# Performance work log

Measured on AMD Instinct MI355X. Metric: run time of the kernel, lower is better.

## Reference

```python
import jax, jax.numpy as jnp
import numpy as np

N = [100000, 25000, 6250]        # nodes per scale (coarsening pyramid)
F = 128                          # features_per_scale (all equal)
H = 4                            # num_heads (only enters via the score scale)
SCALE = float((F // H) ** 0.5)
OUT = 5                          # out_channels
E_SAME = [1000000, 400000, 100000]
E_INC = [400000, 100000]


def _cross_attn(src, dst, src_feat, n_dst, qW, qb, kW, kb, vW, vb):
    # GAT-style gather -> per-edge score -> segment softmax over dst -> scatter.
    # In the original model dst_feat is zeros, so Q = 0 @ qW + qb; we keep the
    # matmul so qW appears in the autodiff graph (its grad is zero, faithfully).
    K = src_feat @ kW + kb
    V = src_feat @ vW + vb
    Q = jnp.zeros((n_dst, qW.shape[1]), src_feat.dtype) @ qW + qb
    score = (Q[dst] * K[src]).sum(-1) / SCALE            # [E]
    m = jax.ops.segment_max(score, dst, num_segments=n_dst)
    e = jnp.exp(score - m[dst])
    denom = jax.ops.segment_sum(e, dst, num_segments=n_dst)
    attn = e / denom[dst]                                # segment softmax
    return jax.ops.segment_sum(attn[:, None] * V[src], dst, num_segments=n_dst)


def _gcn(src, dst, x, n, W, b):
    # DGL GraphConv, norm='both': D_out^-1/2 -> scatter-sum -> D_in^-1/2 -> linear.
    ones = jnp.ones(src.shape[0], x.dtype)
    deg_out = jnp.clip(jax.ops.segment_sum(ones, src, num_segments=n), 1.0)
    deg_in = jnp.clip(jax.ops.segment_sum(ones, dst, num_segments=n), 1.0)
    h = x * jax.lax.rsqrt(deg_out)[:, None]
    agg = jax.ops.segment_sum(h[src], dst, num_segments=n)
    return (agg * jax.lax.rsqrt(deg_in)[:, None]) @ W + b


def setup_inputs() -> dict:
    key = jax.random.key(0)
    cnt = [0]
    def rkey():
        cnt[0] += 1
        return jax.random.fold_in(key, cnt[0])
    def rn(shape, s=0.05):
        return jax.random.normal(rkey(), shape, jnp.float32) * s
    def ri(n, hi):
        return jax.random.randint(rkey(), (n,), 0, hi, jnp.int32)
    return {
        "X": rn((N[0], F), 1.0),
        "emb_W": rn((F, F)), "emb_b": rn((F,)),
        "gcn_W": rn((3, F, F)), "gcn_b": rn((3, F)),
        "enc_qW": rn((2, F, F)), "enc_qb": rn((2, F)),
        "enc_kW": rn((2, F, F)), "enc_kb": rn((2, F)),
        "enc_vW": rn((2, F, F)), "enc_vb": rn((2, F)),
        "dec_qW": rn((2, F, F)), "dec_qb": rn((2, F)),
        "dec_kW": rn((2, F, F)), "dec_kb": rn((2, F)),
        "dec_vW": rn((2, F, F)), "dec_vb": rn((2, F)),
        "head_W": rn((3, 2 * F, OUT)), "head_b": rn((3, OUT)),
        "g0_src": ri(E_SAME[0], N[0]), "g0_dst": ri(E_SAME[0], N[0]),
        "g1_src": ri(E_SAME[1], N[1]), "g1_dst": ri(E_SAME[1], N[1]),
        "g2_src": ri(E_SAME[2], N[2]), "g2_dst": ri(E_SAME[2], N[2]),
        "inc0_src": ri(E_INC[0], N[0]), "inc0_dst": ri(E_INC[0], N[1]),
        "inc1_src": ri(E_INC[1], N[1]), "inc1_dst": ri(E_INC[1], N[2]),
        "dec0_src": ri(E_INC[1], N[2]), "dec0_dst": ri(E_INC[1], N[1]),
        "dec1_src": ri(E_INC[0], N[1]), "dec1_dst": ri(E_INC[0], N[0]),
    }


def reference(X, emb_W, emb_b, gcn_W, gcn_b,
              enc_qW, enc_qb, enc_kW, enc_kb, enc_vW, enc_vb,
              dec_qW, dec_qb, dec_kW, dec_kb, dec_vW, dec_vb,
              head_W, head_b,
              g0_src, g0_dst, g1_src, g1_dst, g2_src, g2_dst,
              inc0_src, inc0_dst, inc1_src, inc1_dst,
              dec0_src, dec0_dst, dec1_src, dec1_dst):
    h0 = X @ emb_W + emb_b                               # embedding, scale 0
    # encoder: scale 0 -> 1 -> 2
    e1 = _cross_attn(inc0_src, inc0_dst, h0, N[1],
                     enc_qW[0], enc_qb[0], enc_kW[0], enc_kb[0], enc_vW[0], enc_vb[0])
    e2 = _cross_attn(inc1_src, inc1_dst, e1, N[2],
                     enc_qW[1], enc_qb[1], enc_kW[1], enc_kb[1], enc_vW[1], enc_vb[1])
    feats = [h0, e1, e2]
    edges = [(g0_src, g0_dst), (g1_src, g1_dst), (g2_src, g2_dst)]
    gcn_out = [_gcn(s, d, feats[i], N[i], gcn_W[i], gcn_b[i])
               for i, (s, d) in enumerate(edges)]
    # decoder: scale 2 -> 1 -> 0
    d1 = _cross_attn(dec0_src, dec0_dst, gcn_out[2], N[1],
                     dec_qW[0], dec_qb[0], dec_kW[0], dec_kb[0], dec_vW[0], dec_vb[0])
    d0 = _cross_attn(dec1_src, dec1_dst, d1, N[0],
                     dec_qW[1], dec_qb[1], dec_kW[1], dec_kb[1], dec_vW[1], dec_vb[1])
    decoded = [d0, d1, gcn_out[2]]
    outs = [jax.nn.softmax(jnp.concatenate([gcn_out[i], decoded[i]], -1) @ head_W[i] + head_b[i], -1)
            for i in range(3)]
    return jnp.concatenate(outs, 0)                      # [N0+N1+N2, OUT]
```

## Files before the change

### kernel.cpp

```cpp
#include <hip/hip_runtime.h>
#include <math.h>

#define N0 100000
#define N1 25000
#define N2 6250
#define FD 128

typedef unsigned short u16;
typedef unsigned int u32;

static inline int ceildiv(int a, int b){ return (a + b - 1)/b; }

__device__ __forceinline__ u16 f2bf(float f){
  u32 u = __float_as_uint(f);
  u += 0x7fffu + ((u >> 16) & 1u);
  return (u16)(u >> 16);
}
__device__ __forceinline__ float bf2f(u16 h){
  return __uint_as_float(((u32)h) << 16);
}
__device__ __forceinline__ float blo(u32 u){ return __uint_as_float(u << 16); }
__device__ __forceinline__ float bhi(u32 u){ return __uint_as_float(u & 0xffff0000u); }
__device__ __forceinline__ u32 pk2(float a, float b){ return (u32)f2bf(a) | ((u32)f2bf(b) << 16); }

struct BMeta {
  const int* src[7]; const int* dst[7];
  int* rowp[7]; int* csr[7];
  int* degp[7];
  int n[7], E[7], B[7], r[7];
  int eoff[8];
  int boff[8];
  int pblk[8];
};

__device__ __forceinline__ void mm_inner(const float* Al, const float* Wl, int r0, int c0, float acc[4][4]){
  #pragma unroll
  for (int kq = 0; kq < 8; ++kq) {
    int k0 = kq*4;
    float4 a[4], w[4];
    #pragma unroll
    for (int i=0;i<4;++i) a[i] = *(const float4*)&Al[(r0+i)*32 + k0];
    #pragma unroll
    for (int kk=0;kk<4;++kk) w[kk] = *(const float4*)&Wl[(k0+kk)*128 + c0];
    #pragma unroll
    for (int i=0;i<4;++i){
      acc[i][0] = fmaf(a[i].x,w[0].x, fmaf(a[i].y,w[1].x, fmaf(a[i].z,w[2].x, fmaf(a[i].w,w[3].x, acc[i][0]))));
      acc[i][1] = fmaf(a[i].x,w[0].y, fmaf(a[i].y,w[1].y, fmaf(a[i].z,w[2].y, fmaf(a[i].w,w[3].y, acc[i][1]))));
      acc[i][2] = fmaf(a[i].x,w[0].z, fmaf(a[i].y,w[1].z, fmaf(a[i].z,w[2].z, fmaf(a[i].w,w[3].z, acc[i][2]))));
      acc[i][3] = fmaf(a[i].x,w[0].w, fmaf(a[i].y,w[1].w, fmaf(a[i].z,w[2].w, fmaf(a[i].w,w[3].w, acc[i][3]))));
    }
  }
}

template<int SCORE, int SCALEDEG, int AB16>
__device__ __forceinline__ void dev_gemm(float* Wl, float* Al, int bid,
    const void* __restrict__ Ap, const int* __restrict__ deg,
    const float* __restrict__ W, const float* __restrict__ bias,
    const float* __restrict__ kvec, float* __restrict__ sOut,
    u16* __restrict__ out, int n)
{
  const int tid = threadIdx.x;
  const int row0 = bid * 32;
  const int c0 = (tid & 31) * 4, r0 = (tid >> 5) * 4;
  const int r = tid >> 3, fc = tid & 7;
  const int gr_s = row0 + r;
  float acc[4][4] = {};
  float sacc = 0.f;
  const float4* W4 = (const float4*)W;
  for (int kp = 0; kp < 4; ++kp) {
    float4* Wl4 = (float4*)Wl;
    #pragma unroll
// ... 18 lines not shown
    mm_inner(Al, Wl, r0, c0, acc);
    __syncthreads();
  }
  if (SCORE){
    sacc += __shfl_xor(sacc, 1);
    sacc += __shfl_xor(sacc, 2);
    sacc += __shfl_xor(sacc, 4);
    if (fc == 0 && gr_s < n) sOut[gr_s] = expf(sacc + kvec[128]);
  }
  float4 bv = make_float4(0.f,0.f,0.f,0.f);
  if (bias) bv = *(const float4*)&bias[c0];
  #pragma unroll
  for (int i=0;i<4;++i){
    int gr = row0 + r0 + i;
    if (gr < n){
      float rs = 1.f;
      if (SCALEDEG) rs = rsqrtf(fmaxf((float)deg[gr], 1.f));
      ushort4 o;
      o.x = f2bf(acc[i][0]*rs+bv.x); o.y = f2bf(acc[i][1]*rs+bv.y);
      o.z = f2bf(acc[i][2]*rs+bv.z); o.w = f2bf(acc[i][3]*rs+bv.w);
      *(ushort4*)&out[(size_t)gr*FD + c0] = o;
    }
  }
}

template<int AB16>
__device__ __forceinline__ void dev_dualgemm(float* sm, int bid,
    const void* __restrict__ Ap, const int* __restrict__ deg,
    const float* __restrict__ Wv, const float* __restrict__ vb,
    const float* __restrict__ Wg,
    const float* __restrict__ kvec, float* __restrict__ sOut,
    u16* __restrict__ Vout, u16* __restrict__ Yout, int n)
{
  float* WvL = sm; float* WgL = sm + 4096; float* Al = sm + 8192;
  const int tid = threadIdx.x;
  const int row0 = bid * 32;
  const int c0 = (tid & 31) * 4, r0 = (tid >> 5) * 4;
  const int r = tid >> 3, fc = tid & 7;
  const int gr_s = row0 + r;
  float accV[4][4] = {};
  float accY[4][4] = {};
  float sacc = 0.f;
  const float4* Wv4 = (const float4*)Wv;
// ... 23 lines not shown
    __syncthreads();
  }
  sacc += __shfl_xor(sacc, 1);
  sacc += __shfl_xor(sacc, 2);
  sacc += __shfl_xor(sacc, 4);
  if (fc == 0 && gr_s < n) sOut[gr_s] = expf(sacc + kvec[128]);
  float4 bv = *(const float4*)&vb[c0];
  #pragma unroll
  for (int i=0;i<4;++i){
    int gr = row0 + r0 + i;
    if (gr < n){
      ushort4 o;
      o.x = f2bf(accV[i][0]+bv.x); o.y = f2bf(accV[i][1]+bv.y);
      o.z = f2bf(accV[i][2]+bv.z); o.w = f2bf(accV[i][3]+bv.w);
      *(ushort4*)&Vout[(size_t)gr*FD + c0] = o;
      float rs = rsqrtf(fmaxf((float)deg[gr], 1.f));
      ushort4 y;
      y.x = f2bf(accY[i][0]*rs); y.y = f2bf(accY[i][1]*rs);
      y.z = f2bf(accY[i][2]*rs); y.w = f2bf(accY[i][3]*rs);
      *(ushort4*)&Yout[(size_t)gr*FD + c0] = y;
    }
  }
}

__device__ __forceinline__ void dev_p0(const BMeta& m, int bid, int* __restrict__ bktCnt, int* sh){
  int j = 0;
  #pragma unroll
  for (int t = 1; t < 7; ++t) if (bid >= m.pblk[t]) j = t;
  int lb = bid - m.pblk[j];
  const int* dst = m.dst[j]; const int* src = m.src[j];
  int* dp = m.degp[j];
  int E = m.E[j], r = m.r[j], B = m.B[j];
  if (threadIdx.x < 64) sh[threadIdx.x] = 0;
  __syncthreads();
  int base = lb*4096 + threadIdx.x;
  #pragma unroll
  for (int i = 0; i < 16; ++i){
    int e = base + i*256;
    if (e < E){
      atomicAdd(&sh[dst[e]/r], 1);
      if (dp) atomicAdd(&dp[src[e]], 1);
    }
  }
  __syncthreads();
  if ((int)threadIdx.x < B) atomicAdd(&bktCnt[m.boff[j] + threadIdx.x], sh[threadIdx.x]);
}

__device__ __forceinline__ void dev_p1(const BMeta& m, const int* __restrict__ bktCnt,
    int* __restrict__ bktBase, int* __restrict__ bktCur, int* sh){
  int tid = threadIdx.x;
  if (tid < 224) sh[tid] = bktCnt[tid];
  __syncthreads();
  if (tid < 7){
    int acc = m.eoff[tid];
    for (int b = m.boff[tid]; b < m.boff[tid+1]; ++b){ int v = sh[b]; sh[b] = acc; acc += v; }
  }
  __syncthreads();
  if (tid < 224){ bktBase[tid] = sh[tid]; bktCur[tid] = sh[tid]; }
}

__device__ __forceinline__ void dev_p2(const BMeta& m, int bid, int* __restrict__ bktCur,
    u32* __restrict__ ebuf, int* sh){
  int j = 0;
  #pragma unroll
  for (int t = 1; t < 7; ++t) if (bid >= m.pblk[t]) j = t;
  int lb = bid - m.pblk[j];
  const int* src = m.src[j]; const int* dst = m.dst[j];
  int E = m.E[j], r = m.r[j], B = m.B[j];
  int* h = sh; int* start = sh + 64;
  if (threadIdx.x < 64) h[threadIdx.x] = 0;
  __syncthreads();
  int base = lb*4096 + threadIdx.x;
  #pragma unroll
  for (int i = 0; i < 16; ++i){ int e = base + i*256; if (e < E) atomicAdd(&h[dst[e]/r], 1); }
  __syncthreads();
  if ((int)threadIdx.x < B) start[threadIdx.x] = atomicAdd(&bktCur[m.boff[j] + threadIdx.x], h[threadIdx.x]);
  __syncthreads();
  #pragma unroll
  for (int i = 0; i < 16; ++i){
    int e = base + i*256;
    if (e < E){
      int s = src[e], d = dst[e];
      int b = d / r;
      int pos = atomicAdd(&start[b], 1);
      ebuf[pos] = ((u32)(d - b*r) << 17) | (u32)s;
    }
  }
}

__device__ __forceinline__ void dev_p3(const BMeta& m, int bb,
    const int* __restrict__ bktCnt, const int* __restrict__ bktBase,
    const u32* __restrict__ ebuf, int* sh){
  int j = 0;
  #pragma unroll
  for (int t = 1; t < 7; ++t) if (bb >= m.boff[t]) j = t;
  int b = bb - m.boff[j];
  int n = m.n[j], r = m.r[j], B = m.B[j];
  int* rowp = m.rowp[j]; int* csr = m.csr[j];
  int node0 = b*r;
  int rr = min(r, n - node0);
  int gbase = bktBase[bb];
  int cnt = bktCnt[bb];
  int lbase = gbase - m.eoff[j];
  int* hist = sh; int* aux = sh + 1568;
  int tid = threadIdx.x;
  for (int i = tid; i < rr; i += 256) hist[i] = 0;
  __syncthreads();
  for (int e = tid; e < cnt; e += 256){ u32 pk = ebuf[gbase + e]; atomicAdd(&hist[pk >> 17], 1); }
  __syncthreads();
  int ch = (rr + 255) >> 8;
  int i0 = tid*ch;
  int s = 0;
  for (int k = 0; k < ch; ++k){ int idx = i0 + k; if (idx < rr){ int t = hist[idx]; hist[idx] = s; s += t; } }
  aux[tid] = s; __syncthreads();
  for (int off = 1; off < 256; off <<= 1){
    int v = aux[tid]; int a = (tid >= off) ? aux[tid - off] : 0;
    __syncthreads();
    aux[tid] = v + a;
    __syncthreads();
  }
// ... 38 lines not shown
    a0*=inv; a1*=inv; a2*=inv; a3*=inv; a4*=inv; a5*=inv; a6*=inv; a7*=inv;
  }
  if (OB16){
    uint4 o; o.x = pk2(a0,a1); o.y = pk2(a2,a3); o.z = pk2(a4,a5); o.w = pk2(a6,a7);
    ((uint4*)out)[(size_t)row*16 + lane] = o;
  } else {
    float4* o4 = (float4*)out;
    o4[(size_t)row*32 + lane*2]     = make_float4(a0,a1,a2,a3);
    o4[(size_t)row*32 + lane*2 + 1] = make_float4(a4,a5,a6,a7);
  }
}

template<int OB16>
__device__ __forceinline__ void dev_gcn_gather16(int bid,
    const int* __restrict__ csr, const int* __restrict__ rowp,
    const u16* __restrict__ Y, const float* __restrict__ bias,
    void* __restrict__ out, int n)
{
  int g = threadIdx.x >> 4, lane = threadIdx.x & 15;
  int row = bid*16 + g;
  if (row >= n) return;
  int st = rowp[row], en = rowp[row+1];
  float a0=0,a1=0,a2=0,a3=0,a4=0,a5=0,a6=0,a7=0;
  const uint4* Y8 = (const uint4*)Y;
  for (int e = st; e < en; ++e){
    int sn = csr[e];
    uint4 v = Y8[(size_t)sn*16 + lane];
    a0 += blo(v.x); a1 += bhi(v.x);
    a2 += blo(v.y); a3 += bhi(v.y);
    a4 += blo(v.z); a5 += bhi(v.z);
    a6 += blo(v.w); a7 += bhi(v.w);
  }
  float sc = rsqrtf(fmaxf((float)(en - st), 1.f));
  const float4* b4 = (const float4*)bias;
  float4 ba = b4[lane*2], bb = b4[lane*2+1];
  float o0=fmaf(a0,sc,ba.x), o1=fmaf(a1,sc,ba.y), o2=fmaf(a2,sc,ba.z), o3=fmaf(a3,sc,ba.w);
  float o4v=fmaf(a4,sc,bb.x), o5=fmaf(a5,sc,bb.y), o6=fmaf(a6,sc,bb.z), o7=fmaf(a7,sc,bb.w);
  if (OB16){
    uint4 o; o.x = pk2(o0,o1); o.y = pk2(o2,o3); o.z = pk2(o4v,o5); o.w = pk2(o6,o7);
    ((uint4*)out)[(size_t)row*16 + lane] = o;
  } else {
    float4* o4 = (float4*)out;
    o4[(size_t)row*32 + lane*2]     = make_float4(o0,o1,o2,o3);
    o4[(size_t)row*32 + lane*2 + 1] = make_float4(o4v,o5,o6,o7);
  }
}
// ... 58 lines not shown
      }
    }
  } else {
    int i = (bid-4)*256 + threadIdx.x;
    if (i < ntot) zeroBlk[i] = 0;
  }
}

__global__ __launch_bounds__(256) void k2_p0_gemm(BMeta m, int* __restrict__ bktCnt,
    const float* __restrict__ X, const float* __restrict__ W, const float* __restrict__ b,
    u16* __restrict__ bh0, int np0)
{
  __shared__ float sm[5120];
  int bid = blockIdx.x;
  if (bid < np0) dev_p0(m, bid, bktCnt, (int*)sm);
  else dev_gemm<0,0,0>(sm, sm+4096, bid - np0, X, nullptr, W, b, nullptr, nullptr, bh0, N0);
}

__global__ __launch_bounds__(256) void k3_p1(BMeta m,
    const int* __restrict__ bktCnt, int* __restrict__ bktBase, int* __restrict__ bktCur)
{
  __shared__ int sh[256];
  dev_p1(m, bktCnt, bktBase, bktCur, sh);
}

__global__ __launch_bounds__(256) void k4_p2_dual(BMeta m, int* __restrict__ bktCur, u32* __restrict__ ebuf,
    const u16* __restrict__ bh0, const int* __restrict__ deg0,
    const float* __restrict__ evW, const float* __restrict__ evb, const float* __restrict__ gW,
    const float* __restrict__ kvec, float* __restrict__ sS, u16* __restrict__ bV, u16* __restrict__ bY0,
    int np2, int gOff)
{
  __shared__ float sm[9216];
  int bid = blockIdx.x;
  if (bid < np2) dev_p2(m, bid, bktCur, ebuf, (int*)sm);
  else dev_dualgemm<1>(sm, gOff + bid - np2, bh0, deg0, evW, evb, gW, kvec, sS, bV, bY0, N0);
}

__global__ __launch_bounds__(256) void k5_p3_dual(BMeta m,
    const int* __restrict__ bktCnt, const int* __restrict__ bktBase, const u32* __restrict__ ebuf,
    const u16* __restrict__ bh0, const int* __restrict__ deg0,
    const float* __restrict__ evW, const float* __restrict__ evb, const float* __restrict__ gW,
    const float* __restrict__ kvec, float* __restrict__ sS, u16* __restrict__ bV, u16* __restrict__ bY0,
    int np3, int gOff)
{
  __shared__ float sm[9216];
  int bid = blockIdx.x;
  if (bid < np3) dev_p3(m, bid, bktCnt, bktBase, ebuf, (int*)sm);
  else dev_dualgemm<1>(sm, gOff + bid - np3, bh0, deg0, evW, evb, gW, kvec, sS, bV, bY0, N0);
}

__global__ __launch_bounds__(256) void k6_ag_i0(
    const int* __restrict__ csrA, const int* __restrict__ rowpA,
    const float* __restrict__ sS, const u16* __restrict__ bV, u16* __restrict__ be1,
    const int* __restrict__ csr0, const int* __restrict__ rowp0, const u16* __restrict__ bY0,
    const float* __restrict__ gb, u16* __restrict__ bg0, int nMain, int sBase)
{
  int bid = blockIdx.x;
  if (bid < nMain) dev_attn_gather16<1>(bid, csrA, rowpA, sS, bV, be1, N1);
  else dev_gcn_gather16<1>(sBase + bid - nMain, csr0, rowp0, bY0, gb, bg0, N0);
}

__global__ __launch_bounds__(256) void k7_dual_enc1(
    const u16* __restrict__ be1, const int* __restrict__ deg1,
    const float* __restrict__ vW, const float* __restrict__ vb, const float* __restrict__ gW,
    const float* __restrict__ kvec, float* __restrict__ sS, u16* __restrict__ bV, u16* __restrict__ bY1,
    const int* __restrict__ csr0, const int* __restrict__ rowp0, const u16* __restrict__ bY0,
    const float* __restrict__ gb, u16* __restrict__ bg0, int nMain, int sBase)
{
  __shared__ float sm[9216];
  int bid = blockIdx.x;
  if (bid < nMain) dev_dualgemm<1>(sm, bid, be1, deg1, vW, vb, gW, kvec, sS, bV, bY1, N1);
  else dev_gcn_gather16<1>(sBase + bid - nMain, csr0, rowp0, bY0, gb, bg0, N0);
}

__global__ __launch_bounds__(256) void k8_ag_i1(
    const int* __restrict__ csrA, const int* __restrict__ rowpA,
    const float* __restrict__ sS, const u16* __restrict__ bV, float* __restrict__ be2,
    const int* __restrict__ csr0, const int* __restrict__ rowp0, const u16* __restrict__ bY0,
    const float* __restrict__ gb, u16* __restrict__ bg0, int nMain, int sBase)
{
  int bid = blockIdx.x;
  if (bid < nMain) dev_attn_gather16<0>(bid, csrA, rowpA, sS, bV, be2, N2);
  else dev_gcn_gather16<1>(sBase + bid - nMain, csr0, rowp0, bY0, gb, bg0, N0);
}

__global__ __launch_bounds__(256) void k9_y2_g1(
    const float* __restrict__ be2, const int* __restrict__ deg2, const float* __restrict__ W2, u16* __restrict__ bY2,
    const int* __restrict__ csr1, const int* __restrict__ rowp1, const u16* __restrict__ bY1,
    const float* __restrict__ b1, u16* __restrict__ bg1,
    const int* __restrict__ csr0, const int* __restrict__ rowp0, const u16* __restrict__ bY0,
    const float* __restrict__ gb, u16* __restrict__ bg0, int ngemm, int nMain, int sBase)
{
  __shared__ float sm[5120];
  int bid = blockIdx.x;
  if (bid < ngemm) dev_gemm<0,1,0>(sm, sm+4096, bid, be2, deg2, W2, nullptr, nullptr, nullptr, bY2, N2);
  else if (bid < nMain) dev_gcn_gather16<1>(bid - ngemm, csr1, rowp1, bY1, b1, bg1, N1);
  else dev_gcn_gather16<1>(sBase + bid - nMain, csr0, rowp0, bY0, gb, bg0, N0);
}

__global__ __launch_bounds__(256) void k10_g2(
    const int* __restrict__ csr2, const int* __restrict__ rowp2, const u16* __restrict__ bY2,
    const float* __restrict__ b2, float* __restrict__ bg2,
    const int* __restrict__ csr0, const int* __restrict__ rowp0, const u16* __restrict__ bY0,
    const float* __restrict__ gb, u16* __restrict__ bg0, int nMain, int sBase)
{
  int bid = blockIdx.x;
  if (bid < nMain) dev_gcn_gather16<0>(bid, csr2, rowp2, bY2, b2, bg2, N2);
  else dev_gcn_gather16<1>(sBase + bid - nMain, csr0, rowp0, bY0, gb, bg0, N0);
}

__global__ __launch_bounds__(256) void k11_dec0_head2(
    const float* __restrict__ bg2, const float* __restrict__ vW, const float* __restrict__ vb,
    const float* __restrict__ kvec, float* __restrict__ sS, u16* __restrict__ bV,
    const float* __restrict__ hW, const float* __restrict__ hb, float* __restrict__ out,
    const int* __restrict__ csr0, const int* __restrict__ rowp0, const u16* __restrict__ bY0,
    const float* __restrict__ gb, u16* __restrict__ bg0, int ngemm, int nMain, int sBase)
{
  __shared__ float sm[5120];
  int bid = blockIdx.x;
  if (bid < ngemm) dev_gemm<1,0,0>(sm, sm+4096, bid, bg2, nullptr, vW, vb, kvec, sS, bV, N2);
  else if (bid < nMain) dev_head<0,0>(bid - ngemm, bg2, bg2, hW, hb, out, N2, N0+N1);
  else dev_gcn_gather16<1>(sBase + bid - nMain, csr0, rowp0, bY0, gb, bg0, N0);
}

__global__ __launch_bounds__(256) void k12_ag_d1(
    const int* __restrict__ csrA, const int* __restrict__ rowpA,
    const float* __restrict__ sS, const u16* __restrict__ bV, u16* __restrict__ be1,
    const int* __restrict__ csr0, const int* __restrict__ rowp0, const u16* __restrict__ bY0,
    const float* __restrict__ gb, u16* __restrict__ bg0, int nMain, int sBase)
{
  int bid = blockIdx.x;
  if (bid < nMain) dev_attn_gather16<1>(bid, csrA, rowpA, sS, bV, be1, N1);
  else dev_gcn_gather16<1>(sBase + bid - nMain, csr0, rowp0, bY0, gb, bg0, N0);
}

__global__ __launch_bounds__(256) void k13_dec1_head1(
    const u16* __restrict__ be1, const float* __restrict__ vW, const float* __restrict__ vb,
    const float* __restrict__ kvec, float* __restrict__ sS, u16* __restrict__ bV,
    const u16* __restrict__ bg1, const float* __restrict__ hW, const float* __restrict__ hb,
    float* __restrict__ out,
    const int* __restrict__ csr0, const int* __restrict__ rowp0, const u16* __restrict__ bY0,
    const float* __restrict__ gb, u16* __restrict__ bg0, int ngemm, int nMain, int sBase)
{
  __shared__ float sm[5120];
  int bid = blockIdx.x;
  if (bid < ngemm) dev_gemm<1,0,1>(sm, sm+4096, bid, be1, nullptr, vW, vb, kvec, sS, bV, N1);
  else if (bid < nMain) dev_head<1,1>(bid - ngemm, bg1, be1, hW, hb, out, N1, N0);
  else dev_gcn_gather16<1>(sBase + bid - nMain, csr0, rowp0, bY0, gb, bg0, N0);
}

__global__ __launch_bounds__(256) void k14_gather_head0(
    const int* __restrict__ csr, const int* __restrict__ rowp,
    const float* __restrict__ w, const u16* __restrict__ V,
    const u16* __restrict__ bg0,
    const float* __restrict__ hW, const float* __restrict__ hb,
    float* __restrict__ out)
{
  int g = threadIdx.x >> 4, lane = threadIdx.x & 15;
  int row = blockIdx.x*16 + g;
  if (row >= N0) return;
  int st = rowp[row], en = rowp[row+1];
  float a0=0,a1=0,a2=0,a3=0,a4=0,a5=0,a6=0,a7=0;
  if (en > st){
// ... 71 lines not shown
  const int* g2d  = (const int*)d_in[24];
  const int* i0s  = (const int*)d_in[25];
  const int* i0d  = (const int*)d_in[26];
  const int* i1s  = (const int*)d_in[27];
  const int* i1d  = (const int*)d_in[28];
  const int* dc0s = (const int*)d_in[29];
  const int* dc0d = (const int*)d_in[30];
  const int* dc1s = (const int*)d_in[31];
  const int* dc1d = (const int*)d_in[32];

  float* ws = (float*)d_ws;
  float* sS  = ws;
  float* kvec = sS + N0;
  float* be2 = kvec + 4*132;
  float* bg2 = be2 + (size_t)N2*FD;
  u16*  bh0 = (u16*)(bg2 + (size_t)N2*FD);
  u16*  be1 = bh0 + (size_t)N0*FD;
  u16*  bg0 = be1 + (size_t)N1*FD;
  u16*  bg1 = bg0 + (size_t)N0*FD;
  u16*  bV  = bg1 + (size_t)N1*FD;
  u16*  bY0 = bV  + (size_t)N0*FD;
  u16*  bY1 = bV + 4000000;
  u16*  bY2 = bV + 8000000;
  int*  degBlk  = (int*)(bY0 + (size_t)N0*FD);
  int*  bktCnt  = degBlk + (N0+N1+N2);
  int*  bktBase = bktCnt + 224;
  int*  bktCur  = bktBase + 224;
  int*  rowpBlk = bktCur + 224;
  int*  csrBlk  = rowpBlk + 287507;
  u32*  ebuf    = (u32*)(csrBlk + 2500000);

  const int* srcP[7] = {g0s,g1s,g2s,i0s,i1s,dc0s,dc1s};
  const int* dstP[7] = {g0d,g1d,g2d,i0d,i1d,dc0d,dc1d};
  const int nArr[7] = {N0,N1,N2,N1,N2,N1,N0};
  const int EArr[7] = {1000000,400000,100000,400000,100000,100000,400000};
  const int BArr[7] = {64,32,8,32,8,16,64};
  const int rArr[7] = {1563,782,782,782,782,1563,1563};
  int* deg0 = degBlk; int* deg1 = degBlk + N0; int* deg2 = degBlk + N0 + N1;
  int* degP[7] = {deg0, deg1, deg2, nullptr, nullptr, nullptr, nullptr};

  BMeta m;
  {
    int eo=0, bo=0, po=0, ro=0, co=0;
    for (int j=0;j<7;++j){
      m.src[j]=srcP[j]; m.dst[j]=dstP[j]; m.degp[j]=degP[j];
      m.rowp[j]=rowpBlk+ro; m.csr[j]=csrBlk+co;
      m.n[j]=nArr[j]; m.E[j]=EArr[j]; m.B[j]=BArr[j]; m.r[j]=rArr[j];
      m.eoff[j]=eo; m.boff[j]=bo; m.pblk[j]=po;
      eo+=EArr[j]; bo+=BArr[j]; po+=ceildiv(EArr[j],4096); ro+=nArr[j]+1; co+=EArr[j];
    }
    m.eoff[7]=eo; m.boff[7]=bo; m.pblk[7]=po;
  }

  const float invScale = 0.17677669529663687f;
  float* out = (float*)d_out;

  const int NP0 = m.pblk[7];
  const int NP3 = m.boff[7];
  const int ZTOT = (N0+N1+N2) + 224;
  const int GH0 = ceildiv(N0,32);
  const int GH1 = ceildiv(N1,32);
  const int GH2 = ceildiv(N2,32);
  const int GS1 = 1250;
  const int GA1_16 = ceildiv(N1,16);
  const int GA2_16 = ceildiv(N2,16);
  const int G0B16  = ceildiv(N0,16);
  const int GH2H = ceildiv(N2,4);
  const int GH1H = ceildiv(N1,4);

  int ss[9];
  for (int i = 0; i <= 8; ++i) ss[i] = (int)(((long long)G0B16 * i) / 8);

  k1_zero_kqv<<<4 + ceildiv(ZTOT,256), 256, 0, stream>>>(degBlk, ZTOT,
      enc_kW, enc_kb, enc_qb, dec_kW, dec_kb, dec_qb, kvec, invScale);
  k2_p0_gemm<<<NP0 + GH0, 256, 0, stream>>>(m, bktCnt, X, emb_W, emb_b, bh0, NP0);
  k3_p1<<<1, 256, 0, stream>>>(m, bktCnt, bktBase, bktCur);
  k4_p2_dual<<<NP0 + GS1, 256, 0, stream>>>(m, bktCur, ebuf,
      bh0, deg0, enc_vW, enc_vb, gcn_W, kvec, sS, bV, bY0, NP0, 0);
  k5_p3_dual<<<NP3 + (GH0 - GS1), 256, 0, stream>>>(m, bktCnt, bktBase, ebuf,
      bh0, deg0, enc_vW, enc_vb, gcn_W, kvec, sS, bV, bY0, NP3, GS1);
  k6_ag_i0<<<GA1_16 + (ss[1]-ss[0]), 256, 0, stream>>>(m.csr[3], m.rowp[3], sS, bV, be1,
      m.csr[0], m.rowp[0], bY0, gcn_b, bg0, GA1_16, ss[0]);
  k7_dual_enc1<<<GH1 + (ss[2]-ss[1]), 256, 0, stream>>>(be1, deg1,
      enc_vW+16384, enc_vb+128, gcn_W+16384, kvec+132, sS, bV, bY1,
      m.csr[0], m.rowp[0], bY0, gcn_b, bg0, GH1, ss[1]);
  k8_ag_i1<<<GA2_16 + (ss[3]-ss[2]), 256, 0, stream>>>(m.csr[4], m.rowp[4], sS, bV, be2,
      m.csr[0], m.rowp[0], bY0, gcn_b, bg0, GA2_16, ss[2]);
  k9_y2_g1<<<GH2 + GA1_16 + (ss[4]-ss[3]), 256, 0, stream>>>(be2, deg2, gcn_W+32768, bY2,
      m.csr[1], m.rowp[1], bY1, gcn_b+128, bg1,
      m.csr[0], m.rowp[0], bY0, gcn_b, bg0, GH2, GH2+GA1_16, ss[3]);
  k10_g2<<<GA2_16 + (ss[5]-ss[4]), 256, 0, stream>>>(m.csr[2], m.rowp[2], bY2, gcn_b+256, bg2,
      m.csr[0], m.rowp[0], bY0, gcn_b, bg0, GA2_16, ss[4]);
  k11_dec0_head2<<<GH2 + GH2H + (ss[6]-ss[5]), 256, 0, stream>>>(bg2, dec_vW, dec_vb, kvec+264, sS, bV,
      head_W+2560, head_b+10, out,
      m.csr[0], m.rowp[0], bY0, gcn_b, bg0, GH2, GH2+GH2H, ss[5]);
  k12_ag_d1<<<GA1_16 + (ss[7]-ss[6]), 256, 0, stream>>>(m.csr[5], m.rowp[5], sS, bV, be1,
      m.csr[0], m.rowp[0], bY0, gcn_b, bg0, GA1_16, ss[6]);
  k13_dec1_head1<<<GH1 + GH1H + (ss[8]-ss[7]), 256, 0, stream>>>(be1, dec_vW+16384, dec_vb+128, kvec+396, sS, bV,
      bg1, head_W+1280, head_b+5, out,
      m.csr[0], m.rowp[0], bY0, gcn_b, bg0, GH1, GH1+GH1H, ss[7]);
  k14_gather_head0<<<G0B16, 256, 0, stream>>>(m.csr[6], m.rowp[6], sS, bV, bg0,
      head_W, head_b, out);
}
```

Measured before the change: 471.6 us.

## Compute out-degree via bucketed shared histograms and apply D_out scaling during GCN gather

Out-degree counting used to rely on global atomicAdd per edge into a degree array. It now reuses the bucket-sort machinery: source keys are binned into 16-bit local indices, and per-bucket shared-memory histograms write rsqrt(out-degree) directly. The GEMM epilogues no longer scale Y by out-degree. Instead the GCN gather multiplies each neighbour row by rs[src] with an FMA, which adds one scalar load per edge. This adds extra binning passes over three edge lists and more scratch buffers, in exchange for removing contended global atomics.

Measured after the change: 457.1 us. -3.1%, faster.

```diff
diff --git a/kernel.cpp b/kernel.cpp
--- a/kernel.cpp
+++ b/kernel.cpp
@@ -24,13 +24,15 @@
 __device__ __forceinline__ u32 pk2(float a, float b){ return (u32)f2bf(a) | ((u32)f2bf(b) << 16); }
 
 struct BMeta {
-  const int* src[7]; const int* dst[7];
+  const int* key[10];
+  const int* src[7];
   int* rowp[7]; int* csr[7];
-  int* degp[7];
-  int n[7], E[7], B[7], r[7];
+  float* rsout[3];
+  int n[10], E[10], B[10], r[10];
   int eoff[8];
-  int boff[8];
-  int pblk[8];
+  int soff[4];
+  int boff[11];
+  int pblk[11];
 };
 
 __device__ __forceinline__ void mm_inner(const float* Al, const float* Wl, int r0, int c0, float acc[4][4]){
@@ -52,9 +54,9 @@
   }
 }
 
-template<int SCORE, int SCALEDEG, int AB16>
+template<int SCORE, int AB16>
 __device__ __forceinline__ void dev_gemm(float* Wl, float* Al, int bid,
-    const void* __restrict__ Ap, const int* __restrict__ deg,
+    const void* __restrict__ Ap,
     const float* __restrict__ W, const float* __restrict__ bias,
     const float* __restrict__ kvec, float* __restrict__ sOut,
     u16* __restrict__ out, int n)
@@ -103,11 +105,9 @@
   for (int i=0;i<4;++i){
     int gr = row0 + r0 + i;
     if (gr < n){
-      float rs = 1.f;
-      if (SCALEDEG) rs = rsqrtf(fmaxf((float)deg[gr], 1.f));
       ushort4 o;
-      o.x = f2bf(acc[i][0]*rs+bv.x); o.y = f2bf(acc[i][1]*rs+bv.y);
-      o.z = f2bf(acc[i][2]*rs+bv.z); o.w = f2bf(acc[i][3]*rs+bv.w);
+      o.x = f2bf(acc[i][0]+bv.x); o.y = f2bf(acc[i][1]+bv.y);
+      o.z = f2bf(acc[i][2]+bv.z); o.w = f2bf(acc[i][3]+bv.w);
       *(ushort4*)&out[(size_t)gr*FD + c0] = o;
     }
   }
@@ -115,7 +115,7 @@
 
 template<int AB16>
 __device__ __forceinline__ void dev_dualgemm(float* sm, int bid,
-    const void* __restrict__ Ap, const int* __restrict__ deg,
+    const void* __restrict__ Ap,
     const float* __restrict__ Wv, const float* __restrict__ vb,
     const float* __restrict__ Wg,
     const float* __restrict__ kvec, float* __restrict__ sOut,
@@ -169,34 +169,30 @@
       o.x = f2bf(accV[i][0]+bv.x); o.y = f2bf(accV[i][1]+bv.y);
       o.z = f2bf(accV[i][2]+bv.z); o.w = f2bf(accV[i][3]+bv.w);
       *(ushort4*)&Vout[(size_t)gr*FD + c0] = o;
-      float rs = rsqrtf(fmaxf((float)deg[gr], 1.f));
       ushort4 y;
-      y.x = f2bf(accY[i][0]*rs); y.y = f2bf(accY[i][1]*rs);
-      y.z = f2bf(accY[i][2]*rs); y.w = f2bf(accY[i][3]*rs);
+      y.x = f2bf(accY[i][0]); y.y = f2bf(accY[i][1]);
+      y.z = f2bf(accY[i][2]); y.w = f2bf(accY[i][3]);
       *(ushort4*)&Yout[(size_t)gr*FD + c0] = y;
     }
   }
 }
 
+__device__ __forceinline__ int job_of_blk(const BMeta& m, int bid){
+  int j = 0;
+  #pragma unroll
+  for (int t = 1; t < 10; ++t) if (bid >= m.pblk[t]) j = t;
+  return j;
+}
+
 __device__ __forceinline__ void dev_p0(const BMeta& m, int bid, int* __restrict__ bktCnt, int* sh){
-  int j = 0;
-  #pragma unroll
-  for (int t = 1; t < 7; ++t) if (bid >= m.pblk[t]) j = t;
+  int j = job_of_blk(m, bid);
   int lb = bid - m.pblk[j];
-  const int* dst = m.dst[j]; const int* src = m.src[j];
-  int* dp = m.degp[j];
-  int E = m.E[j], r = m.r[j], B = m.B[j];
+  const int* key = m.key[j]; int E = m.E[j], r = m.r[j], B = m.B[j];
   if (threadIdx.x < 64) sh[threadIdx.x] = 0;
   __syncthreads();
   int base = lb*4096 + threadIdx.x;
   #pragma unroll
-  for (int i = 0; i < 16; ++i){
-    int e = base + i*256;
-    if (e < E){
-      atomicAdd(&sh[dst[e]/r], 1);
-      if (dp) atomicAdd(&dp[src[e]], 1);
-    }
-  }
+  for (int i = 0; i < 16; ++i){ int e = base + i*256; if (e < E) atomicAdd(&sh[key[e]/r], 1); }
   __syncthreads();
   if ((int)threadIdx.x < B) atomicAdd(&bktCnt[m.boff[j] + threadIdx.x], sh[threadIdx.x]);
 }
@@ -204,61 +200,84 @@
 __device__ __forceinline__ void dev_p1(const BMeta& m, const int* __restrict__ bktCnt,
     int* __restrict__ bktBase, int* __restrict__ bktCur, int* sh){
   int tid = threadIdx.x;
-  if (tid < 224) sh[tid] = bktCnt[tid];
-  __syncthreads();
-  if (tid < 7){
-    int acc = m.eoff[tid];
+  for (int i = tid; i < 328; i += 256) sh[i] = bktCnt[i];
+  __syncthreads();
+  if (tid < 10){
+    int acc = (tid < 7) ? m.eoff[tid] : m.soff[tid-7];
     for (int b = m.boff[tid]; b < m.boff[tid+1]; ++b){ int v = sh[b]; sh[b] = acc; acc += v; }
   }
   __syncthreads();
-  if (tid < 224){ bktBase[tid] = sh[tid]; bktCur[tid] = sh[tid]; }
+  for (int i = tid; i < 328; i += 256){ bktBase[i] = sh[i]; bktCur[i] = sh[i]; }
 }
 
 __device__ __forceinline__ void dev_p2(const BMeta& m, int bid, int* __restrict__ bktCur,
-    u32* __restrict__ ebuf, int* sh){
-  int j = 0;
-  #pragma unroll
-  for (int t = 1; t < 7; ++t) if (bid >= m.pblk[t]) j = t;
+    u32* __restrict__ ebuf, u16* __restrict__ ebuf16, int* sh){
+  int j = job_of_blk(m, bid);
   int lb = bid - m.pblk[j];
-  const int* src = m.src[j]; const int* dst = m.dst[j];
+  const int* key = m.key[j];
   int E = m.E[j], r = m.r[j], B = m.B[j];
   int* h = sh; int* start = sh + 64;
   if (threadIdx.x < 64) h[threadIdx.x] = 0;
   __syncthreads();
   int base = lb*4096 + threadIdx.x;
   #pragma unroll
-  for (int i = 0; i < 16; ++i){ int e = base + i*256; if (e < E) atomicAdd(&h[dst[e]/r], 1); }
+  for (int i = 0; i < 16; ++i){ int e = base + i*256; if (e < E) atomicAdd(&h[key[e]/r], 1); }
   __syncthreads();
   if ((int)threadIdx.x < B) start[threadIdx.x] = atomicAdd(&bktCur[m.boff[j] + threadIdx.x], h[threadIdx.x]);
   __syncthreads();
-  #pragma unroll
-  for (int i = 0; i < 16; ++i){
-    int e = base + i*256;
-    if (e < E){
-      int s = src[e], d = dst[e];
-      int b = d / r;
-      int pos = atomicAdd(&start[b], 1);
-      ebuf[pos] = ((u32)(d - b*r) << 17) | (u32)s;
+  if (j < 7){
+    const int* src = m.src[j];
+    #pragma unroll
+    for (int i = 0; i < 16; ++i){
+      int e = base + i*256;
+      if (e < E){
+        int s = src[e], d = key[e];
+        int b = d / r;
+        int pos = atomicAdd(&start[b], 1);
+        ebuf[pos] = ((u32)(d - b*r) << 17) | (u32)s;
+      }
+    }
+  } else {
+    #pragma unroll
+    for (int i = 0; i < 16; ++i){
+      int e = base + i*256;
+      if (e < E){
+        int k = key[e];
+        int b = k / r;
+        int pos = atomicAdd(&start[b], 1);
+        ebuf16[pos] = (u16)(k - b*r);
+      }
     }
   }
 }
 
 __device__ __forceinline__ void dev_p3(const BMeta& m, int bb,
     const int* __restrict__ bktCnt, const int* __restrict__ bktBase,
-    const u32* __restrict__ ebuf, int* sh){
+    const u32* __restrict__ ebuf, const u16* __restrict__ ebuf16, int* sh){
   int j = 0;
   #pragma unroll
-  for (int t = 1; t < 7; ++t) if (bb >= m.boff[t]) j = t;
+  for (int t = 1; t < 10; ++t) if (bb >= m.boff[t]) j = t;
   int b = bb - m.boff[j];
-  int n = m.n[j], r = m.r[j], B = m.B[j];
-  int* rowp = m.rowp[j]; int* csr = m.csr[j];
+  int n = m.n[j], r = m.r[j];
   int node0 = b*r;
   int rr = min(r, n - node0);
   int gbase = bktBase[bb];
   int cnt = bktCnt[bb];
+  int tid = threadIdx.x;
+  if (j >= 7){
+    int* hist = sh;
+    for (int i = tid; i < rr; i += 256) hist[i] = 0;
+    __syncthreads();
+    for (int e = tid; e < cnt; e += 256) atomicAdd(&hist[ebuf16[gbase + e]], 1);
+    __syncthreads();
+    float* rs = m.rsout[j-7];
+    for (int i = tid; i < rr; i += 256) rs[node0 + i] = rsqrtf(fmaxf((float)hist[i], 1.f));
+    return;
+  }
+  int B = m.B[j];
+  int* rowp = m.rowp[j]; int* csr = m.csr[j];
   int lbase = gbase - m.eoff[j];
   int* hist = sh; int* aux = sh + 1568;
-  int tid = threadIdx.x;
   for (int i = tid; i < rr; i += 256) hist[i] = 0;
   __syncthreads();
   for (int e = tid; e < cnt; e += 256){ u32 pk = ebuf[gbase + e]; atomicAdd(&hist[pk >> 17], 1); }
@@ -327,8 +346,8 @@
 template<int OB16>
 __device__ __forceinline__ void dev_gcn_gather16(int bid,
     const int* __restrict__ csr, const int* __restrict__ rowp,
-    const u16* __restrict__ Y, const float* __restrict__ bias,
-    void* __restrict__ out, int n)
+    const float* __restrict__ rs, const u16* __restrict__ Y,
+    const float* __restrict__ bias, void* __restrict__ out, int n)
 {
   int g = threadIdx.x >> 4, lane = threadIdx.x & 15;
   int row = bid*16 + g;
@@ -338,11 +357,12 @@
   const uint4* Y8 = (const uint4*)Y;
   for (int e = st; e < en; ++e){
     int sn = csr[e];
+    float x = rs[sn];
     uint4 v = Y8[(size_t)sn*16 + lane];
-    a0 += blo(v.x); a1 += bhi(v.x);
-    a2 += blo(v.y); a3 += bhi(v.y);
-    a4 += blo(v.z); a5 += bhi(v.z);
-    a6 += blo(v.w); a7 += bhi(v.w);
+    a0 = fmaf(x, blo(v.x), a0); a1 = fmaf(x, bhi(v.x), a1);
+    a2 = fmaf(x, blo(v.y), a2); a3 = fmaf(x, bhi(v.y), a3);
+    a4 = fmaf(x, blo(v.z), a4); a5 = fmaf(x, bhi(v.z), a5);
+    a6 = fmaf(x, blo(v.w), a6); a7 = fmaf(x, bhi(v.w), a7);
   }
   float sc = rsqrtf(fmaxf((float)(en - st), 1.f));
   const float4* b4 = (const float4*)bias;
@@ -431,124 +451,128 @@
   __shared__ float sm[5120];
   int bid = blockIdx.x;
   if (bid < np0) dev_p0(m, bid, bktCnt, (int*)sm);
-  else dev_gemm<0,0,0>(sm, sm+4096, bid - np0, X, nullptr, W, b, nullptr, nullptr, bh0, N0);
+  else dev_gemm<0,0>(sm, sm+4096, bid - np0, X, W, b, nullptr, nullptr, bh0, N0);
 }
 
 __global__ __launch_bounds__(256) void k3_p1(BMeta m,
     const int* __restrict__ bktCnt, int* __restrict__ bktBase, int* __restrict__ bktCur)
 {
-  __shared__ int sh[256];
+  __shared__ int sh[384];
   dev_p1(m, bktCnt, bktBase, bktCur, sh);
 }
 
-__global__ __launch_bounds__(256) void k4_p2_dual(BMeta m, int* __restrict__ bktCur, u32* __restrict__ ebuf,
-    const u16* __restrict__ bh0, const int* __restrict__ deg0,
+__global__ __launch_bounds__(256) void k4_p2_dual(BMeta m, int* __restrict__ bktCur,
+    u32* __restrict__ ebuf, u16* __restrict__ ebuf16,
+    const u16* __restrict__ bh0,
     const float* __restrict__ evW, const float* __restrict__ evb, const float* __restrict__ gW,
     const float* __restrict__ kvec, float* __restrict__ sS, u16* __restrict__ bV, u16* __restrict__ bY0,
     int np2, int gOff)
 {
   __shared__ float sm[9216];
   int bid = blockIdx.x;
-  if (bid < np2) dev_p2(m, bid, bktCur, ebuf, (int*)sm);
-  else dev_dualgemm<1>(sm, gOff + bid - np2, bh0, deg0, evW, evb, gW, kvec, sS, bV, bY0, N0);
+  if (bid < np2) dev_p2(m, bid, bktCur, ebuf, ebuf16, (int*)sm);
+  else dev_dualgemm<1>(sm, gOff + bid - np2, bh0, evW, evb, gW, kvec, sS, bV, bY0, N0);
 }
 
 __global__ __launch_bounds__(256) void k5_p3_dual(BMeta m,
-    const int* __restrict__ bktCnt, const int* __restrict__ bktBase, const u32* __restrict__ ebuf,
-    const u16* __restrict__ bh0, const int* __restrict__ deg0,
+    const int* __restrict__ bktCnt, const int* __restrict__ bktBase,
+    const u32* __restrict__ ebuf, const u16* __restrict__ ebuf16,
+    const u16* __restrict__ bh0,
     const float* __restrict__ evW, const float* __restrict__ evb, const float* __restrict__ gW,
     const float* __restrict__ kvec, float* __restrict__ sS, u16* __restrict__ bV, u16* __restrict__ bY0,
     int np3, int gOff)
 {
   __shared__ float sm[9216];
   int bid = blockIdx.x;
-  if (bid < np3) dev_p3(m, bid, bktCnt, bktBase, ebuf, (int*)sm);
-  else dev_dualgemm<1>(sm, gOff + bid - np3, bh0, deg0, evW, evb, gW, kvec, sS, bV, bY0, N0);
+  if (bid < np3) dev_p3(m, bid, bktCnt, bktBase, ebuf, ebuf16, (int*)sm);
+  else dev_dualgemm<1>(sm, gOff + bid - np3, bh0, evW, evb, gW, kvec, sS, bV, bY0, N0);
 }
 
 __global__ __launch_bounds__(256) void k6_ag_i0(
     const int* __restrict__ csrA, const int* __restrict__ rowpA,
     const float* __restrict__ sS, const u16* __restrict__ bV, u16* __restrict__ be1,
-    const int* __restrict__ csr0, const int* __restrict__ rowp0, const u16* __restrict__ bY0,
-    const float* __restrict__ gb, u16* __restrict__ bg0, int nMain, int sBase)
+    const int* __restrict__ csr0, const int* __restrict__ rowp0, const float* __restrict__ rs0,
+    const u16* __restrict__ bY0, const float* __restrict__ gb, u16* __restrict__ bg0, int nMain, int sBase)
 {
   int bid = blockIdx.x;
   if (bid < nMain) dev_attn_gather16<1>(bid, csrA, rowpA, sS, bV, be1, N1);
-  else dev_gcn_gather16<1>(sBase + bid - nMain, csr0, rowp0, bY0, gb, bg0, N0);
+  else dev_gcn_gather16<1>(sBase + bid - nMain, csr0, rowp0, rs0, bY0, gb, bg0, N0);
 }
 
 __global__ __launch_bounds__(256) void k7_dual_enc1(
-    const u16* __restrict__ be1, const int* __restrict__ deg1,
+    const u16* __restrict__ be1,
     const float* __restrict__ vW, const float* __restrict__ vb, const float* __restrict__ gW,
     const float* __restrict__ kvec, float* __restrict__ sS, u16* __restrict__ bV, u16* __restrict__ bY1,
-    const int* __restrict__ csr0, const int* __restrict__ rowp0, const u16* __restrict__ bY0,
-    const float* __restrict__ gb, u16* __restrict__ bg0, int nMain, int sBase)
+    const int* __restrict__ csr0, const int* __restrict__ rowp0, const float* __restrict__ rs0,
+    const u16* __restrict__ bY0, const float* __restrict__ gb, u16* __restrict__ bg0, int nMain, int sBase)
 {
   __shared__ float sm[9216];
   int bid = blockIdx.x;
-  if (bid < nMain) dev_dualgemm<1>(sm, bid, be1, deg1, vW, vb, gW, kvec, sS, bV, bY1, N1);
-  else dev_gcn_gather16<1>(sBase + bid - nMain, csr0, rowp0, bY0, gb, bg0, N0);
+  if (bid < nMain) dev_dualgemm<1>(sm, bid, be1, vW, vb, gW, kvec, sS, bV, bY1, N1);
+  else dev_gcn_gather16<1>(sBase + bid - nMain, csr0, rowp0, rs0, bY0, gb, bg0, N0);
 }
 
 __global__ __launch_bounds__(256) void k8_ag_i1(
     const int* __restrict__ csrA, const int* __restrict__ rowpA,
     const float* __restrict__ sS, const u16* __restrict__ bV, float* __restrict__ be2,
-    const int* __restrict__ csr0, const int* __restrict__ rowp0, const u16* __restrict__ bY0,
-    const float* __restrict__ gb, u16* __restrict__ bg0, int nMain, int sBase)
+    const int* __restrict__ csr0, const int* __restrict__ rowp0, const float* __restrict__ rs0,
+    const u16* __restrict__ bY0, const float* __restrict__ gb, u16* __restrict__ bg0, int nMain, int sBase)
 {
   int bid = blockIdx.x;
   if (bid < nMain) dev_attn_gather16<0>(bid, csrA, rowpA, sS, bV, be2, N2);
-  else dev_gcn_gather16<1>(sBase + bid - nMain, csr0, rowp0, bY0, gb, bg0, N0);
+  else dev_gcn_gather16<1>(sBase + bid - nMain, csr0, rowp0, rs0, bY0, gb, bg0, N0);
 }
 
 __global__ __launch_bounds__(256) void k9_y2_g1(
-    const float* __restrict__ be2, const int* __restrict__ deg2, const float* __restrict__ W2, u16* __restrict__ bY2,
-    const int* __restrict__ csr1, const int* __restrict__ rowp1, const u16* __restrict__ bY1,
-    const float* __restrict__ b1, u16* __restrict__ bg1,
-    const int* __restrict__ csr0, const int* __restrict__ rowp0, const u16* __restrict__ bY0,
-    const float* __restrict__ gb, u16* __restrict__ bg0, int ngemm, int nMain, int sBase)
+    const float* __restrict__ be2, const float* __restrict__ W2, u16* __restrict__ bY2,
+    const int* __restrict__ csr1, const int* __restrict__ rowp1, const float* __restrict__ rs1,
+    const u16* __restrict__ bY1, const float* __restrict__ b1, u16* __restrict__ bg1,
+    const int* __restrict__ csr0, const int* __restrict__ rowp0, const float* __restrict__ rs0,
+    const u16* __restrict__ bY0, const float* __restrict__ gb, u16* __restrict__ bg0,
+    int ngemm, int nMain, int sBase)
 {
   __shared__ float sm[5120];
   int bid = blockIdx.x;
-  if (bid < ngemm) dev_gemm<0,1,0>(sm, sm+4096, bid, be2, deg2, W2, nullptr, nullptr, nullptr, bY2, N2);
-  else if (bid < nMain) dev_gcn_gather16<1>(bid - ngemm, csr1, rowp1, bY1, b1, bg1, N1);
-  else dev_gcn_gather16<1>(sBase + bid - nMain, csr0, rowp0, bY0, gb, bg0, N0);
+  if (bid < ngemm) dev_gemm<0,0>(sm, sm+4096, bid, be2, W2, nullptr, nullptr, nullptr, bY2, N2);
+  else if (bid < nMain) dev_gcn_gather16<1>(bid - ngemm, csr1, rowp1, rs1, bY1, b1, bg1, N1);
+  else dev_gcn_gather16<1>(sBase + bid - nMain, csr0, rowp0, rs0, bY0, gb, bg0, N0);
 }
 
 __global__ __launch_bounds__(256) void k10_g2(
-    const int* __restrict__ csr2, const int* __restrict__ rowp2, const u16* __restrict__ bY2,
-    const float* __restrict__ b2, float* __restrict__ bg2,
-    const int* __restrict__ csr0, const int* __restrict__ rowp0, const u16* __restrict__ bY0,
-    const float* __restrict__ gb, u16* __restrict__ bg0, int nMain, int sBase)
-{
-  int bid = blockIdx.x;
-  if (bid < nMain) dev_gcn_gather16<0>(bid, csr2, rowp2, bY2, b2, bg2, N2);
-  else dev_gcn_gather16<1>(sBase + bid - nMain, csr0, rowp0, bY0, gb, bg0, N0);
+    const int* __restrict__ csr2, const int* __restrict__ rowp2, const float* __restrict__ rs2,
+    const u16* __restrict__ bY2, const float* __restrict__ b2, float* __restrict__ bg2,
+    const int* __restrict__ csr0, const int* __restrict__ rowp0, const float* __restrict__ rs0,
+    const u16* __restrict__ bY0, const float* __restrict__ gb, u16* __restrict__ bg0, int nMain, int sBase)
+{
+  int bid = blockIdx.x;
+  if (bid < nMain) dev_gcn_gather16<0>(bid, csr2, rowp2, rs2, bY2, b2, bg2, N2);
+  else dev_gcn_gather16<1>(sBase + bid - nMain, csr0, rowp0, rs0, bY0, gb, bg0, N0);
 }
 
 __global__ __launch_bounds__(256) void k11_dec0_head2(
     const float* __restrict__ bg2, const float* __restrict__ vW, const float* __restrict__ vb,
     const float* __restrict__ kvec, float* __restrict__ sS, u16* __restrict__ bV,
     const float* __restrict__ hW, const float* __restrict__ hb, float* __restrict__ out,
-    const int* __restrict__ csr0, const int* __restrict__ rowp0, const u16* __restrict__ bY0,
-    const float* __restrict__ gb, u16* __restrict__ bg0, int ngemm, int nMain, int sBase)
+    const int* __restrict__ csr0, const int* __restrict__ rowp0, const float* __restrict__ rs0,
+    const u16* __restrict__ bY0, const float* __restrict__ gb, u16* __restrict__ bg0,
+    int ngemm, int nMain, int sBase)
 {
   __shared__ float sm[5120];
   int bid = blockIdx.x;
-  if (bid < ngemm) dev_gemm<1,0,0>(sm, sm+4096, bid, bg2, nullptr, vW, vb, kvec, sS, bV, N2);
+  if (bid < ngemm) dev_gemm<1,0>(sm, sm+4096, bid, bg2, vW, vb, kvec, sS, bV, N2);
   else if (bid < nMain) dev_head<0,0>(bid - ngemm, bg2, bg2, hW, hb, out, N2, N0+N1);
-  else dev_gcn_gather16<1>(sBase + bid - nMain, csr0, rowp0, bY0, gb, bg0, N0);
+  else dev_gcn_gather16<1>(sBase + bid - nMain, csr0, rowp0, rs0, bY0, gb, bg0, N0);
 }
 
 __global__ __launch_bounds__(256) void k12_ag_d1(
     const int* __restrict__ csrA, const int* __restrict__ rowpA,
     const float* __restrict__ sS, const u16* __restrict__ bV, u16* __restrict__ be1,
-    const int* __restrict__ csr0, const int* __restrict__ rowp0, const u16* __restrict__ bY0,
-    const float* __restrict__ gb, u16* __restrict__ bg0, int nMain, int sBase)
+    const int* __restrict__ csr0, const int* __restrict__ rowp0, const float* __restrict__ rs0,
+    const u16* __restrict__ bY0, const float* __restrict__ gb, u16* __restrict__ bg0, int nMain, int sBase)
 {
   int bid = blockIdx.x;
   if (bid < nMain) dev_attn_gather16<1>(bid, csrA, rowpA, sS, bV, be1, N1);
-  else dev_gcn_gather16<1>(sBase + bid - nMain, csr0, rowp0, bY0, gb, bg0, N0);
+  else dev_gcn_gather16<1>(sBase + bid - nMain, csr0, rowp0, rs0, bY0, gb, bg0, N0);
 }
 
 __global__ __launch_bounds__(256) void k13_dec1_head1(
@@ -556,14 +580,15 @@
     const float* __restrict__ kvec, float* __restrict__ sS, u16* __restrict__ bV,
     const u16* __restrict__ bg1, const float* __restrict__ hW, const float* __restrict__ hb,
     float* __restrict__ out,
-    const int* __restrict__ csr0, const int* __restrict__ rowp0, const u16* __restrict__ bY0,
-    const float* __restrict__ gb, u16* __restrict__ bg0, int ngemm, int nMain, int sBase)
+    const int* __restrict__ csr0, const int* __restrict__ rowp0, const float* __restrict__ rs0,
+    const u16* __restrict__ bY0, const float* __restrict__ gb, u16* __restrict__ bg0,
+    int ngemm, int nMain, int sBase)
 {
   __shared__ float sm[5120];
   int bid = blockIdx.x;
-  if (bid < ngemm) dev_gemm<1,0,1>(sm, sm+4096, bid, be1, nullptr, vW, vb, kvec, sS, bV, N1);
+  if (bid < ngemm) dev_gemm<1,1>(sm, sm+4096, bid, be1, vW, vb, kvec, sS, bV, N1);
   else if (bid < nMain) dev_head<1,1>(bid - ngemm, bg1, be1, hW, hb, out, N1, N0);
-  else dev_gcn_gather16<1>(sBase + bid - nMain, csr0, rowp0, bY0, gb, bg0, N0);
+  else dev_gcn_gather16<1>(sBase + bid - nMain, csr0, rowp0, rs0, bY0, gb, bg0, N0);
 }
 
 __global__ __launch_bounds__(256) void k14_gather_head0(
@@ -665,7 +690,10 @@
   float* kvec = sS + N0;
   float* be2 = kvec + 4*132;
   float* bg2 = be2 + (size_t)N2*FD;
-  u16*  bh0 = (u16*)(bg2 + (size_t)N2*FD);
+  float* rs0 = bg2 + (size_t)N2*FD;
+  float* rs1 = rs0 + N0;
+  float* rs2 = rs1 + N1;
+  u16*  bh0 = (u16*)(rs2 + N2 + 2);
   u16*  be1 = bh0 + (size_t)N0*FD;
   u16*  bg0 = be1 + (size_t)N1*FD;
   u16*  bg1 = bg0 + (size_t)N0*FD;
@@ -673,42 +701,45 @@
   u16*  bY0 = bV  + (size_t)N0*FD;
   u16*  bY1 = bV + 4000000;
   u16*  bY2 = bV + 8000000;
-  int*  degBlk  = (int*)(bY0 + (size_t)N0*FD);
-  int*  bktCnt  = degBlk + (N0+N1+N2);
-  int*  bktBase = bktCnt + 224;
-  int*  bktCur  = bktBase + 224;
-  int*  rowpBlk = bktCur + 224;
+  int*  bktCnt  = (int*)(bY0 + (size_t)N0*FD);
+  int*  bktBase = bktCnt + 328;
+  int*  bktCur  = bktBase + 328;
+  int*  rowpBlk = bktCur + 328;
   int*  csrBlk  = rowpBlk + 287507;
   u32*  ebuf    = (u32*)(csrBlk + 2500000);
-
-  const int* srcP[7] = {g0s,g1s,g2s,i0s,i1s,dc0s,dc1s};
-  const int* dstP[7] = {g0d,g1d,g2d,i0d,i1d,dc0d,dc1d};
-  const int nArr[7] = {N0,N1,N2,N1,N2,N1,N0};
-  const int EArr[7] = {1000000,400000,100000,400000,100000,100000,400000};
-  const int BArr[7] = {64,32,8,32,8,16,64};
-  const int rArr[7] = {1563,782,782,782,782,1563,1563};
-  int* deg0 = degBlk; int* deg1 = degBlk + N0; int* deg2 = degBlk + N0 + N1;
-  int* degP[7] = {deg0, deg1, deg2, nullptr, nullptr, nullptr, nullptr};
+  u16*  ebuf16  = (u16*)(ebuf + 2500000);
+
+  const int* keyP[10] = {g0d,g1d,g2d,i0d,i1d,dc0d,dc1d, g0s,g1s,g2s};
+  const int* srcP[7]  = {g0s,g1s,g2s,i0s,i1s,dc0s,dc1s};
+  const int nArr[10] = {N0,N1,N2,N1,N2,N1,N0, N0,N1,N2};
+  const int EArr[10] = {1000000,400000,100000,400000,100000,100000,400000, 1000000,400000,100000};
+  const int BArr[10] = {64,32,8,32,8,16,64, 64,32,8};
+  const int rArr[10] = {1563,782,782,782,782,1563,1563, 1563,782,782};
 
   BMeta m;
   {
-    int eo=0, bo=0, po=0, ro=0, co=0;
-    for (int j=0;j<7;++j){
-      m.src[j]=srcP[j]; m.dst[j]=dstP[j]; m.degp[j]=degP[j];
-      m.rowp[j]=rowpBlk+ro; m.csr[j]=csrBlk+co;
+    int eo=0, so=0, bo=0, po=0, ro=0, co=0;
+    for (int j=0;j<10;++j){
+      m.key[j]=keyP[j];
       m.n[j]=nArr[j]; m.E[j]=EArr[j]; m.B[j]=BArr[j]; m.r[j]=rArr[j];
-      m.eoff[j]=eo; m.boff[j]=bo; m.pblk[j]=po;
-      eo+=EArr[j]; bo+=BArr[j]; po+=ceildiv(EArr[j],4096); ro+=nArr[j]+1; co+=EArr[j];
-    }
-    m.eoff[7]=eo; m.boff[7]=bo; m.pblk[7]=po;
-  }
+      m.boff[j]=bo; m.pblk[j]=po;
+      bo+=BArr[j]; po+=ceildiv(EArr[j],4096);
+      if (j < 7){
+        m.src[j]=srcP[j]; m.rowp[j]=rowpBlk+ro; m.csr[j]=csrBlk+co;
+        m.eoff[j]=eo; eo+=EArr[j]; ro+=nArr[j]+1; co+=EArr[j];
+      } else {
+        m.soff[j-7]=so; so+=EArr[j];
+      }
+    }
+    m.eoff[7]=eo; m.soff[3]=so; m.boff[10]=bo; m.pblk[10]=po;
+  }
+  m.rsout[0]=rs0; m.rsout[1]=rs1; m.rsout[2]=rs2;
 
   const float invScale = 0.17677669529663687f;
   float* out = (float*)d_out;
 
-  const int NP0 = m.pblk[7];
-  const int NP3 = m.boff[7];
-  const int ZTOT = (N0+N1+N2) + 224;
+  const int NP = m.pblk[10];
+  const int NB = m.boff[10];
   const int GH0 = ceildiv(N0,32);
   const int GH1 = ceildiv(N1,32);
   const int GH2 = ceildiv(N2,32);
@@ -722,34 +753,34 @@
   int ss[9];
   for (int i = 0; i <= 8; ++i) ss[i] = (int)(((long long)G0B16 * i) / 8);
 
-  k1_zero_kqv<<<4 + ceildiv(ZTOT,256), 256, 0, stream>>>(degBlk, ZTOT,
+  k1_zero_kqv<<<4 + ceildiv(NB,256), 256, 0, stream>>>(bktCnt, NB,
       enc_kW, enc_kb, enc_qb, dec_kW, dec_kb, dec_qb, kvec, invScale);
-  k2_p0_gemm<<<NP0 + GH0, 256, 0, stream>>>(m, bktCnt, X, emb_W, emb_b, bh0, NP0);
+  k2_p0_gemm<<<NP + GH0, 256, 0, stream>>>(m, bktCnt, X, emb_W, emb_b, bh0, NP);
   k3_p1<<<1, 256, 0, stream>>>(m, bktCnt, bktBase, bktCur);
-  k4_p2_dual<<<NP0 + GS1, 256, 0, stream>>>(m, bktCur, ebuf,
-      bh0, deg0, enc_vW, enc_vb, gcn_W, kvec, sS, bV, bY0, NP0, 0);
-  k5_p3_dual<<<NP3 + (GH0 - GS1), 256, 0, stream>>>(m, bktCnt, bktBase, ebuf,
-      bh0, deg0, enc_vW, enc_vb, gcn_W, kvec, sS, bV, bY0, NP3, GS1);
+  k4_p2_dual<<<NP + GS1, 256, 0, stream>>>(m, bktCur, ebuf, ebuf16,
+      bh0, enc_vW, enc_vb, gcn_W, kvec, sS, bV, bY0, NP, 0);
+  k5_p3_dual<<<NB + (GH0 - GS1), 256, 0, stream>>>(m, bktCnt, bktBase, ebuf, ebuf16,
+      bh0, enc_vW, enc_vb, gcn_W, kvec, sS, bV, bY0, NB, GS1);
   k6_ag_i0<<<GA1_16 + (ss[1]-ss[0]), 256, 0, stream>>>(m.csr[3], m.rowp[3], sS, bV, be1,
-      m.csr[0], m.rowp[0], bY0, gcn_b, bg0, GA1_16, ss[0]);
-  k7_dual_enc1<<<GH1 + (ss[2]-ss[1]), 256, 0, stream>>>(be1, deg1,
+      m.csr[0], m.rowp[0], rs0, bY0, gcn_b, bg0, GA1_16, ss[0]);
+  k7_dual_enc1<<<GH1 + (ss[2]-ss[1]), 256, 0, stream>>>(be1,
       enc_vW+16384, enc_vb+128, gcn_W+16384, kvec+132, sS, bV, bY1,
-      m.csr[0], m.rowp[0], bY0, gcn_b, bg0, GH1, ss[1]);
+      m.csr[0], m.rowp[0], rs0, bY0, gcn_b, bg0, GH1, ss[1]);
   k8_ag_i1<<<GA2_16 + (ss[3]-ss[2]), 256, 0, stream>>>(m.csr[4], m.rowp[4], sS, bV, be2,
-      m.csr[0], m.rowp[0], bY0, gcn_b, bg0, GA2_16, ss[2]);
-  k9_y2_g1<<<GH2 + GA1_16 + (ss[4]-ss[3]), 256, 0, stream>>>(be2, deg2, gcn_W+32768, bY2,
-      m.csr[1], m.rowp[1], bY1, gcn_b+128, bg1,
-      m.csr[0], m.rowp[0], bY0, gcn_b, bg0, GH2, GH2+GA1_16, ss[3]);
-  k10_g2<<<GA2_16 + (ss[5]-ss[4]), 256, 0, stream>>>(m.csr[2], m.rowp[2], bY2, gcn_b+256, bg2,
-      m.csr[0], m.rowp[0], bY0, gcn_b, bg0, GA2_16, ss[4]);
+      m.csr[0], m.rowp[0], rs0, bY0, gcn_b, bg0, GA2_16, ss[2]);
+  k9_y2_g1<<<GH2 + GA1_16 + (ss[4]-ss[3]), 256, 0, stream>>>(be2, gcn_W+32768, bY2,
+      m.csr[1], m.rowp[1], rs1, bY1, gcn_b+128, bg1,
+      m.csr[0], m.rowp[0], rs0, bY0, gcn_b, bg0, GH2, GH2+GA1_16, ss[3]);
+  k10_g2<<<GA2_16 + (ss[5]-ss[4]), 256, 0, stream>>>(m.csr[2], m.rowp[2], rs2, bY2, gcn_b+256, bg2,
+      m.csr[0], m.rowp[0], rs0, bY0, gcn_b, bg0, GA2_16, ss[4]);
   k11_dec0_head2<<<GH2 + GH2H + (ss[6]-ss[5]), 256, 0, stream>>>(bg2, dec_vW, dec_vb, kvec+264, sS, bV,
       head_W+2560, head_b+10, out,
-      m.csr[0], m.rowp[0], bY0, gcn_b, bg0, GH2, GH2+GH2H, ss[5]);
+      m.csr[0], m.rowp[0], rs0, bY0, gcn_b, bg0, GH2, GH2+GH2H, ss[5]);
   k12_ag_d1<<<GA1_16 + (ss[7]-ss[6]), 256, 0, stream>>>(m.csr[5], m.rowp[5], sS, bV, be1,
-      m.csr[0], m.rowp[0], bY0, gcn_b, bg0, GA1_16, ss[6]);
+      m.csr[0], m.rowp[0], rs0, bY0, gcn_b, bg0, GA1_16, ss[6]);
   k13_dec1_head1<<<GH1 + GH1H + (ss[8]-ss[7]), 256, 0, stream>>>(be1, dec_vW+16384, dec_vb+128, kvec+396, sS, bV,
       bg1, head_W+1280, head_b+5, out,
-      m.csr[0], m.rowp[0], bY0, gcn_b, bg0, GH1, GH1+GH1H, ss[7]);
+      m.csr[0], m.rowp[0], rs0, bY0, gcn_b, bg0, GH1, GH1+GH1H, ss[7]);
   k14_gather_head0<<<G0B16, 256, 0, stream>>>(m.csr[6], m.rowp[6], sS, bV, bg0,
       head_W, head_b, out);
 }
```
